# Kernel optimization log

Measured on AMD Instinct MI355X. Metric: run time of the kernel, lower is better.

The kernel has to match this reference:

```python
import jax, jax.numpy as jnp
import numpy as np

N, H, T, G = 4096, 64, 6, 16  # nodes, hidden, topk kvecs, graphs


def _rope(h, pos, kvecs, batch):
    # h: [N,H], pos: [N,3], kvecs: [G,T,3], batch: [N]
    phase = jnp.einsum('nc,ntc->nt', pos, kvecs[batch])      # [N,T]
    cos = jnp.cos(phase).T[:, :, None]                        # [T,N,1]
    sin = jnp.sin(phase).T[:, :, None]
    a, b = h[:, 0::2], h[:, 1::2]                             # [N,H/2] each
    rot_a = a[None] * cos - b[None] * sin                     # [T,N,H/2]
    rot_b = a[None] * sin + b[None] * cos
    return jnp.concatenate([rot_a, rot_b], axis=-1)           # [T,N,H]


def setup_inputs() -> dict:
    key = jax.random.key(0)
    ks = jax.random.split(key, 8)
    node_feat = jax.random.normal(ks[0], (N, H), dtype=jnp.float32)
    node_feat_sr = jax.random.normal(ks[1], (N, H), dtype=jnp.float32)
    positions = jax.random.uniform(ks[2], (N, 3), dtype=jnp.float32) * 12.0  # ~bulk-water box
    kvecs = jax.random.normal(ks[3], (G, T, 3), dtype=jnp.float32)
    batch = jnp.sort(jax.random.randint(ks[4], (N,), 0, G)).astype(jnp.int32)
    W_readout = jax.random.normal(ks[5], (H, H), dtype=jnp.float32) / np.sqrt(H)
    W_qkv = jax.random.normal(ks[6], (3 * H, H), dtype=jnp.float32) / np.sqrt(H)
    W_tp = jax.random.normal(ks[7], (H, H, H), dtype=jnp.float32) / H
    return {'node_feat': node_feat, 'node_feat_sr': node_feat_sr,
            'positions': positions, 'kvecs': kvecs, 'batch': batch,
            'W_readout': W_readout, 'W_qkv': W_qkv, 'W_tp': W_tp}


def reference(node_feat, node_feat_sr, positions, kvecs, batch, W_readout, W_qkv, W_tp):
    scale_q = 1.0 / np.sqrt(H)
    scalars = node_feat @ W_readout.T                         # linear_readout -> [N,H]
    qkv = scalars @ W_qkv.T                                   # [N,3H]
    q, k, v = qkv[:, :H], qkv[:, H:2 * H], qkv[:, 2 * H:]
    q, k = jax.nn.silu(q), jax.nn.silu(k)
    q = _rope(q, positions, kvecs, batch) * scale_q           # [T,N,H]
    k = _rope(k, positions, kvecs, batch)                     # [T,N,H]
    # per-node outer product k (x) v, scatter-summed per graph
    kv_node = k[:, :, :, None] * v[None, :, None, :]          # [T,N,H,H]
    kv_graph = jax.ops.segment_sum(kv_node.transpose(1, 0, 2, 3), batch,
                                   num_segments=G)            # [G,T,H,H]
    # beta[t,n,e] = sum_d q[t,n,d] * kv_graph[batch[n],t,d,e]; update = beta.sum(0)
    update = jnp.einsum('tnd,ntde->ne', q, kv_graph[batch])   # [N,H]
    # FullyConnectedTensorProduct(Hx0e, Hx0e -> Hx0e) == bilinear form
    node_nl = jnp.einsum('ni,nj,kij->nk', node_feat_sr, update, W_tp)
    return node_nl
```

## Files before the change

kernel.cpp:

```cpp
#include <hip/hip_runtime.h>

#define NN 4096
#define HH 64
#define TT 6
#define GG 16

constexpr int OFF_OFFS = 0;
constexpr int OFF_QS   = 32;
constexpr int OFF_KS   = OFF_QS + NN * HH;
constexpr int OFF_VS   = OFF_KS + NN * HH;
constexpr int OFF_COS  = OFF_VS + NN * HH;
constexpr int OFF_SIN  = OFF_COS + NN * 8;
constexpr int OFF_KVG  = OFF_SIN + NN * 8;
constexpr int OFF_UPD  = OFF_KVG + GG * TT * HH * HH;

typedef __bf16 bf16x8 __attribute__((ext_vector_type(8)));
typedef float f32x4 __attribute__((ext_vector_type(4)));

__global__ __launch_bounds__(256) void k_qkv(const float* __restrict__ feat,
                                             const float* __restrict__ pos,
                                             const float* __restrict__ kvecs,
                                             const int* __restrict__ batch,
                                             const float* __restrict__ Wro,
                                             const float* __restrict__ Wqkv,
                                             float* __restrict__ ws) {
    int tid = threadIdx.x, blk = blockIdx.x;
    if (blk == 256) {
        int g = tid;
        if (g <= GG) {
            int lo = 0, hi = NN;
            while (lo < hi) { int mid = (lo + hi) >> 1; if (batch[mid] < g) lo = mid + 1; else hi = mid; }
            ((int*)(ws + OFF_OFFS))[g] = lo;
        }
        return;
    }
    {
        float4 z = {0.f, 0.f, 0.f, 0.f};
        float4* kz = (float4*)(ws + OFF_KVG) + blk * 384;
        kz[tid] = z;
        if (tid < 128) kz[256 + tid] = z;
    }
    __shared__ float Wro_l[64][66];
    __shared__ float Wq_l[192][66];
    #pragma unroll
    for (int k = 0; k < 16; ++k) {
        int idx = k * 256 + tid;
        Wro_l[idx >> 6][idx & 63] = Wro[idx];
    }
    #pragma unroll
    for (int k = 0; k < 48; ++k) {
        int idx = k * 256 + tid;
        Wq_l[idx >> 6][idx & 63] = Wqkv[idx];
    }
    __syncthreads();
    int w = tid >> 6, j = tid & 63;
    float fl[4];
    #pragma unroll
    for (int mi = 0; mi < 4; ++mi) fl[mi] = feat[(blk * 16 + w * 4 + mi) * 64 + j];
    float scal[4] = {0.f, 0.f, 0.f, 0.f};
    #pragma unroll
    for (int i4 = 0; i4 < 16; ++i4) {
        float4 w4 = *(const float4*)&Wro_l[j][i4 * 4];
        #pragma unroll
        for (int mi = 0; mi < 4; ++mi) {
            scal[mi] += __shfl(fl[mi], i4 * 4 + 0, 64) * w4.x
                      + __shfl(fl[mi], i4 * 4 + 1, 64) * w4.y
                      + __shfl(fl[mi], i4 * 4 + 2, 64) * w4.z
                      + __shfl(fl[mi], i4 * 4 + 3, 64) * w4.w;
        }
    }
    float qa[4] = {0.f,0.f,0.f,0.f}, ka[4] = {0.f,0.f,0.f,0.f}, va[4] = {0.f,0.f,0.f,0.f};
    #pragma unroll
    for (int i4 = 0; i4 < 16; ++i4) {
        float4 wq = *(const float4*)&Wq_l[j][i4 * 4];
        float4 wk = *(const float4*)&Wq_l[64 + j][i4 * 4];
        float4 wv = *(const float4*)&Wq_l[128 + j][i4 * 4];
        #pragma unroll
        for (int mi = 0; mi < 4; ++mi) {
            float s0 = __shfl(scal[mi], i4 * 4 + 0, 64);
            float s1 = __shfl(scal[mi], i4 * 4 + 1, 64);
            float s2 = __shfl(scal[mi], i4 * 4 + 2, 64);
            float s3 = __shfl(scal[mi], i4 * 4 + 3, 64);
            qa[mi] += s0 * wq.x + s1 * wq.y + s2 * wq.z + s3 * wq.w;
            ka[mi] += s0 * wk.x + s1 * wk.y + s2 * wk.z + s3 * wk.w;
            va[mi] += s0 * wv.x + s1 * wv.y + s2 * wv.z + s3 * wv.w;
        }
    }
    #pragma unroll
    for (int mi = 0; mi < 4; ++mi) {
        int n = blk * 16 + w * 4 + mi;
        float q = qa[mi], kk2 = ka[mi], v = va[mi];
        float qs = q / (1.f + __expf(-q)) * 0.125f;
        float ks = kk2 / (1.f + __expf(-kk2));
        ws[OFF_QS + n * 64 + j] = qs;
        ws[OFF_KS + n * 64 + j] = ks;
        ws[OFF_VS + n * 64 + j] = v;
        if (j < 6) {
            int g = batch[n];
            const float* kv = &kvecs[(g * 6 + j) * 3];
            float ph = pos[n * 3 + 0] * kv[0] + pos[n * 3 + 1] * kv[1] + pos[n * 3 + 2] * kv[2];
            ws[OFF_COS + n * 8 + j] = cosf(ph);
            ws[OFF_SIN + n * 8 + j] = sinf(ph);
        }
    }
}

__global__ __launch_bounds__(256) void k_kvg(float* __restrict__ ws) {
    __shared__ float kr8[8][64];
    __shared__ float v8[8][64];
    int bid = blockIdx.x;
    int g = bid / 48, rem = bid % 48, t = rem >> 3, ch = rem & 7;
    const int* off = (const int*)(ws + OFF_OFFS);
    int n0 = off[g] + ch * 64;
    int n1 = min(off[g + 1], n0 + 64);
    if (n0 >= n1) return;
    int tid = threadIdx.x;
    int e = tid & 63, dg = tid >> 6;
    float acc[16];
    #pragma unroll
    for (int k = 0; k < 16; ++k) acc[k] = 0.f;
    for (int base = n0; base < n1; base += 8) {
        int cnt = min(8, n1 - base);
        #pragma unroll
        for (int half = 0; half < 2; ++half) {
            int idx = half * 256 + tid;
            int ns = idx >> 6, d = idx & 63;
            float kr = 0.f, vv = 0.f;
            if (ns < cnt) {
                int n = base + ns;
                float ka2 = ws[OFF_KS + n * 64 + 2 * (d & 31)];
                float kb = ws[OFF_KS + n * 64 + 2 * (d & 31) + 1];
                float c = ws[OFF_COS + n * 8 + t], s = ws[OFF_SIN + n * 8 + t];
                kr = (d < 32) ? (ka2 * c - kb * s) : (ka2 * s + kb * c);
                vv = ws[OFF_VS + n * 64 + d];
            }
            kr8[ns][d] = kr; v8[ns][d] = vv;
        }
        __syncthreads();
        #pragma unroll
        for (int ns = 0; ns < 8; ++ns) {
            float vv = v8[ns][e];
            const float4* kp = (const float4*)&kr8[ns][dg * 16];
            #pragma unroll
            for (int q4 = 0; q4 < 4; ++q4) {
                float4 kq = kp[q4];
                acc[q4 * 4 + 0] += kq.x * vv; acc[q4 * 4 + 1] += kq.y * vv;
                acc[q4 * 4 + 2] += kq.z * vv; acc[q4 * 4 + 3] += kq.w * vv;
            }
        }
        __syncthreads();
    }
    float* kvg = ws + OFF_KVG + ((g * 6 + t) * 64 + dg * 16) * 64;
    #pragma unroll
    for (int k = 0; k < 16; ++k) atomicAdd(&kvg[k * 64 + e], acc[k]);
}

__global__ __launch_bounds__(256) void k_upd(float* __restrict__ ws, float* __restrict__ out) {
    int tid = threadIdx.x, bid = blockIdx.x;
    ((float4*)out)[bid * 256 + tid] = (float4){0.f, 0.f, 0.f, 0.f};
    int g = bid >> 4, ch = bid & 15;
    const int* off = (const int*)(ws + OFF_OFFS);
    int n0 = off[g] + ch * 32;
    int nend = off[g + 1];
    if (n0 >= nend) return;
    int w = tid >> 6, lane = tid & 63;
    int wm = w & 1, wn = w >> 1;
    int lr = lane & 15, lg = lane >> 4;
    int nrow = n0 + wm * 16 + lr;
    int nc = min(nrow, nend - 1);
    float qv[16];
    const float* qsr = ws + OFF_QS + nc * 64 + lg * 16;
    #pragma unroll
    for (int u = 0; u < 4; ++u) *(float4*)&qv[u * 4] = *(const float4*)&qsr[u * 4];
    float cs[8], sn[8];
    *(float4*)&cs[0] = *(const float4*)(ws + OFF_COS + nc * 8);
    *(float4*)&cs[4] = *(const float4*)(ws + OFF_COS + nc * 8 + 4);
    *(float4*)&sn[0] = *(const float4*)(ws + OFF_SIN + nc * 8);
    *(float4*)&sn[4] = *(const float4*)(ws + OFF_SIN + nc * 8 + 4);
    const float* kvg = ws + OFF_KVG + g * (TT * HH * HH);
    int col0 = wn * 32 + lr, col1 = col0 + 16;
    f32x4 acc0 = {0.f,0.f,0.f,0.f}, acc1 = {0.f,0.f,0.f,0.f};
    #pragma unroll
    for (int kk = 0; kk < 12; ++kk) {
        int t = kk >> 1;
        float c = cs[t], s = sn[t];
        bf16x8 afr;
        #pragma unroll
        for (int ii = 0; ii < 8; ++ii) {
            float a = qv[2 * ii], b = qv[2 * ii + 1];
            float r = ((kk & 1) == 0) ? (a * c - b * s) : (a * s + b * c);
            afr[ii] = (__bf16)r;
        }
        const float* bp = kvg + (kk * 32 + lg * 8) * 64;
        bf16x8 b0, b1;
        #pragma unroll
        for (int i = 0; i < 8; ++i) {
            b0[i] = (__bf16)bp[i * 64 + col0];
            b1[i] = (__bf16)bp[i * 64 + col1];
        }
        acc0 = __builtin_amdgcn_mfma_f32_16x16x32_bf16(afr, b0, acc0, 0, 0, 0);
        acc1 = __builtin_amdgcn_mfma_f32_16x16x32_bf16(afr, b1, acc1, 0, 0, 0);
    }
    #pragma unroll
    for (int r = 0; r < 4; ++r) {
        int n = n0 + wm * 16 + lg * 4 + r;
        if (n < nend) {
            ws[OFF_UPD + n * 64 + col0] = acc0[r];
            ws[OFF_UPD + n * 64 + col1] = acc1[r];
        }
    }
}

__device__ __forceinline__ bf16x8 make_afrag(const float* p, float s) {
    float4 u0 = *(const float4*)p;
    float4 u1 = *(const float4*)(p + 4);
    bf16x8 r;
    r[0] = (__bf16)(s * u0.x); r[1] = (__bf16)(s * u0.y); r[2] = (__bf16)(s * u0.z); r[3] = (__bf16)(s * u0.w);
    r[4] = (__bf16)(s * u1.x); r[5] = (__bf16)(s * u1.y); r[6] = (__bf16)(s * u1.z); r[7] = (__bf16)(s * u1.w);
    return r;
}
__device__ __forceinline__ bf16x8 make_bfrag(const float* p) {
    float4 u0 = *(const float4*)p;
    float4 u1 = *(const float4*)(p + 4);
    bf16x8 r;
    r[0] = (__bf16)u0.x; r[1] = (__bf16)u0.y; r[2] = (__bf16)u0.z; r[3] = (__bf16)u0.w;
    r[4] = (__bf16)u1.x; r[5] = (__bf16)u1.y; r[6] = (__bf16)u1.z; r[7] = (__bf16)u1.w;
    return r;
}

__global__ __launch_bounds__(256) void k_out(const float* __restrict__ sr,
                                             const float* __restrict__ Wtp,
                                             const float* __restrict__ ws,
                                             float* __restrict__ out) {
    __shared__ float sr_l[64][65];
    __shared__ float up_l[64][68];
    __shared__ float w_l[64][68];
    int tid = threadIdx.x;
    int mb = blockIdx.x & 63, kspl = blockIdx.x >> 6;
    int m0 = mb * 64;
    #pragma unroll
    for (int k = 0; k < 16; ++k) {
        int idx = k * 256 + tid;
        int m = idx >> 6, c = idx & 63;
        sr_l[m][c] = sr[(m0 + m) * 64 + c];
        up_l[m][c] = ws[OFF_UPD + (m0 + m) * 64 + c];
    }
    __syncthreads();
    int w = tid >> 6, lane = tid & 63;
    int wm = w >> 1, wn = w & 1;
    int lr = lane & 15, lg = lane >> 4;
    f32x4 acc[2][2];
    #pragma unroll
    for (int a = 0; a < 2; ++a)
        #pragma unroll
        for (int b = 0; b < 2; ++b) acc[a][b] = (f32x4){0.f, 0.f, 0.f, 0.f};

    for (int ii = 0; ii < 8; ++ii) {
        int i = kspl * 8 + ii;
        #pragma unroll
        for (int k = 0; k < 4; ++k) {
            int idx = k * 256 + tid;
            int col = idx >> 4, j4 = (idx & 15) * 4;
            float4 wv = *(const float4*)&Wtp[(col * 64 + i) * 64 + j4];
            *(float4*)&w_l[col][j4] = wv;
        }
        __syncthreads();
        float s0 = sr_l[wm * 32 + lr][i];
        float s1 = sr_l[wm * 32 + 16 + lr][i];
        #pragma unroll
        for (int kc = 0; kc < 2; ++kc) {
            int j0 = kc * 32 + lg * 8;
            bf16x8 a0 = make_afrag(&up_l[wm * 32 + lr][j0], s0);
            bf16x8 a1 = make_afrag(&up_l[wm * 32 + 16 + lr][j0], s1);
            bf16x8 b0 = make_bfrag(&w_l[wn * 32 + lr][j0]);
            bf16x8 b1 = make_bfrag(&w_l[wn * 32 + 16 + lr][j0]);
            acc[0][0] = __builtin_amdgcn_mfma_f32_16x16x32_bf16(a0, b0, acc[0][0], 0, 0, 0);
            acc[0][1] = __builtin_amdgcn_mfma_f32_16x16x32_bf16(a0, b1, acc[0][1], 0, 0, 0);
            acc[1][0] = __builtin_amdgcn_mfma_f32_16x16x32_bf16(a1, b0, acc[1][0], 0, 0, 0);
            acc[1][1] = __builtin_amdgcn_mfma_f32_16x16x32_bf16(a1, b1, acc[1][1], 0, 0, 0);
        }
        __syncthreads();
    }
    #pragma unroll
    for (int mt = 0; mt < 2; ++mt)
        #pragma unroll
        for (int nt = 0; nt < 2; ++nt) {
            int row = m0 + wm * 32 + mt * 16 + lg * 4;
            int col = wn * 32 + nt * 16 + lr;
            #pragma unroll
            for (int r = 0; r < 4; ++r)
                atomicAdd(&out[(row + r) * 64 + col], acc[mt][nt][r]);
        }
}

extern "C" void kernel_launch(void* const* d_in, const int* in_sizes, int n_in,
                              void* d_out, int out_size, void* d_ws, size_t ws_size,
                              hipStream_t stream) {
    const float* node_feat    = (const float*)d_in[0];
    const float* node_feat_sr = (const float*)d_in[1];
    const float* positions    = (const float*)d_in[2];
    const float* kvecs        = (const float*)d_in[3];
    const int*   batch        = (const int*)d_in[4];
    const float* W_readout    = (const float*)d_in[5];
    const float* W_qkv        = (const float*)d_in[6];
    const float* W_tp         = (const float*)d_in[7];
    float* out = (float*)d_out;
    float* ws  = (float*)d_ws;

    k_qkv<<<257, 256, 0, stream>>>(node_feat, positions, kvecs, batch, W_readout, W_qkv, ws);
    k_kvg<<<768, 256, 0, stream>>>(ws);
    k_upd<<<256, 256, 0, stream>>>(ws, out);
    k_out<<<512, 256, 0, stream>>>(node_feat_sr, W_tp, ws, out);
}
```

Measured before the change: 126.1 us.

## Rebalance grid sizes across kernels and move output zeroing into kvg kernel

Doubles the k_qkv grid so each block handles 8 nodes instead of 16, and halves the KV-graph zeroing per block to match. k_upd now uses 16-node chunks with one MFMA tile per wave, giving twice as many blocks, and k_out halves its block count by giving each block twice as many i-slices. Output zeroing moves from k_upd into k_kvg. The aim is better occupancy and load balance in the early kernels and fewer atomics in k_out. The cost is re-staging the weights into shared memory in more blocks and longer serial loops in k_out.

```diff
diff --git a/kernel.cpp b/kernel.cpp
--- a/kernel.cpp
+++ b/kernel.cpp
@@ -25,7 +25,7 @@
                                              const float* __restrict__ Wqkv,
                                              float* __restrict__ ws) {
     int tid = threadIdx.x, blk = blockIdx.x;
-    if (blk == 256) {
+    if (blk == 512) {
         int g = tid;
         if (g <= GG) {
             int lo = 0, hi = NN;
@@ -34,11 +34,9 @@
         }
         return;
     }
-    {
-        float4 z = {0.f, 0.f, 0.f, 0.f};
-        float4* kz = (float4*)(ws + OFF_KVG) + blk * 384;
-        kz[tid] = z;
-        if (tid < 128) kz[256 + tid] = z;
+    if (tid < 192) {
+        float4* kz = (float4*)(ws + OFF_KVG) + blk * 192;
+        kz[tid] = (float4){0.f, 0.f, 0.f, 0.f};
     }
     __shared__ float Wro_l[64][66];
     __shared__ float Wq_l[192][66];
@@ -54,29 +52,29 @@
     }
     __syncthreads();
     int w = tid >> 6, j = tid & 63;
-    float fl[4];
-    #pragma unroll
-    for (int mi = 0; mi < 4; ++mi) fl[mi] = feat[(blk * 16 + w * 4 + mi) * 64 + j];
-    float scal[4] = {0.f, 0.f, 0.f, 0.f};
+    float fl[2];
+    #pragma unroll
+    for (int mi = 0; mi < 2; ++mi) fl[mi] = feat[(blk * 8 + w * 2 + mi) * 64 + j];
+    float scal[2] = {0.f, 0.f};
     #pragma unroll
     for (int i4 = 0; i4 < 16; ++i4) {
         float4 w4 = *(const float4*)&Wro_l[j][i4 * 4];
         #pragma unroll
-        for (int mi = 0; mi < 4; ++mi) {
+        for (int mi = 0; mi < 2; ++mi) {
             scal[mi] += __shfl(fl[mi], i4 * 4 + 0, 64) * w4.x
                       + __shfl(fl[mi], i4 * 4 + 1, 64) * w4.y
                       + __shfl(fl[mi], i4 * 4 + 2, 64) * w4.z
                       + __shfl(fl[mi], i4 * 4 + 3, 64) * w4.w;
         }
     }
-    float qa[4] = {0.f,0.f,0.f,0.f}, ka[4] = {0.f,0.f,0.f,0.f}, va[4] = {0.f,0.f,0.f,0.f};
+    float qa[2] = {0.f,0.f}, ka[2] = {0.f,0.f}, va[2] = {0.f,0.f};
     #pragma unroll
     for (int i4 = 0; i4 < 16; ++i4) {
         float4 wq = *(const float4*)&Wq_l[j][i4 * 4];
         float4 wk = *(const float4*)&Wq_l[64 + j][i4 * 4];
         float4 wv = *(const float4*)&Wq_l[128 + j][i4 * 4];
         #pragma unroll
-        for (int mi = 0; mi < 4; ++mi) {
+        for (int mi = 0; mi < 2; ++mi) {
             float s0 = __shfl(scal[mi], i4 * 4 + 0, 64);
             float s1 = __shfl(scal[mi], i4 * 4 + 1, 64);
             float s2 = __shfl(scal[mi], i4 * 4 + 2, 64);
@@ -87,8 +85,8 @@
         }
     }
     #pragma unroll
-    for (int mi = 0; mi < 4; ++mi) {
-        int n = blk * 16 + w * 4 + mi;
+    for (int mi = 0; mi < 2; ++mi) {
+        int n = blk * 8 + w * 2 + mi;
         float q = qa[mi], kk2 = ka[mi], v = va[mi];
         float qs = q / (1.f + __expf(-q)) * 0.125f;
         float ks = kk2 / (1.f + __expf(-kk2));
@@ -105,16 +103,19 @@
     }
 }
 
-__global__ __launch_bounds__(256) void k_kvg(float* __restrict__ ws) {
+__global__ __launch_bounds__(256) void k_kvg(float* __restrict__ ws, float* __restrict__ out) {
     __shared__ float kr8[8][64];
     __shared__ float v8[8][64];
     int bid = blockIdx.x;
+    int tid = threadIdx.x;
+    if (bid < 256) {
+        ((float4*)out)[bid * 256 + tid] = (float4){0.f, 0.f, 0.f, 0.f};
+    }
     int g = bid / 48, rem = bid % 48, t = rem >> 3, ch = rem & 7;
     const int* off = (const int*)(ws + OFF_OFFS);
     int n0 = off[g] + ch * 64;
     int n1 = min(off[g + 1], n0 + 64);
     if (n0 >= n1) return;
-    int tid = threadIdx.x;
     int e = tid & 63, dg = tid >> 6;
     float acc[16];
     #pragma unroll
@@ -155,18 +156,16 @@
     for (int k = 0; k < 16; ++k) atomicAdd(&kvg[k * 64 + e], acc[k]);
 }
 
-__global__ __launch_bounds__(256) void k_upd(float* __restrict__ ws, float* __restrict__ out) {
+__global__ __launch_bounds__(256) void k_upd(float* __restrict__ ws) {
     int tid = threadIdx.x, bid = blockIdx.x;
-    ((float4*)out)[bid * 256 + tid] = (float4){0.f, 0.f, 0.f, 0.f};
-    int g = bid >> 4, ch = bid & 15;
+    int g = bid >> 5, ch = bid & 31;
     const int* off = (const int*)(ws + OFF_OFFS);
-    int n0 = off[g] + ch * 32;
+    int n0 = off[g] + ch * 16;
     int nend = off[g + 1];
     if (n0 >= nend) return;
     int w = tid >> 6, lane = tid & 63;
-    int wm = w & 1, wn = w >> 1;
     int lr = lane & 15, lg = lane >> 4;
-    int nrow = n0 + wm * 16 + lr;
+    int nrow = n0 + lr;
     int nc = min(nrow, nend - 1);
     float qv[16];
     const float* qsr = ws + OFF_QS + nc * 64 + lg * 16;
@@ -178,8 +177,8 @@
     *(float4*)&sn[0] = *(const float4*)(ws + OFF_SIN + nc * 8);
     *(float4*)&sn[4] = *(const float4*)(ws + OFF_SIN + nc * 8 + 4);
     const float* kvg = ws + OFF_KVG + g * (TT * HH * HH);
-    int col0 = wn * 32 + lr, col1 = col0 + 16;
-    f32x4 acc0 = {0.f,0.f,0.f,0.f}, acc1 = {0.f,0.f,0.f,0.f};
+    int col0 = w * 16 + lr;
+    f32x4 acc0 = {0.f,0.f,0.f,0.f};
     #pragma unroll
     for (int kk = 0; kk < 12; ++kk) {
         int t = kk >> 1;
@@ -192,22 +191,15 @@
             afr[ii] = (__bf16)r;
         }
         const float* bp = kvg + (kk * 32 + lg * 8) * 64;
-        bf16x8 b0, b1;
-        #pragma unroll
-        for (int i = 0; i < 8; ++i) {
-            b0[i] = (__bf16)bp[i * 64 + col0];
-            b1[i] = (__bf16)bp[i * 64 + col1];
-        }
+        bf16x8 b0;
+        #pragma unroll
+        for (int i = 0; i < 8; ++i) b0[i] = (__bf16)bp[i * 64 + col0];
         acc0 = __builtin_amdgcn_mfma_f32_16x16x32_bf16(afr, b0, acc0, 0, 0, 0);
-        acc1 = __builtin_amdgcn_mfma_f32_16x16x32_bf16(afr, b1, acc1, 0, 0, 0);
     }
     #pragma unroll
     for (int r = 0; r < 4; ++r) {
-        int n = n0 + wm * 16 + lg * 4 + r;
-        if (n < nend) {
-            ws[OFF_UPD + n * 64 + col0] = acc0[r];
-            ws[OFF_UPD + n * 64 + col1] = acc1[r];
-        }
+        int n = n0 + lg * 4 + r;
+        if (n < nend) ws[OFF_UPD + n * 64 + col0] = acc0[r];
     }
 }
 
@@ -255,8 +247,8 @@
         #pragma unroll
         for (int b = 0; b < 2; ++b) acc[a][b] = (f32x4){0.f, 0.f, 0.f, 0.f};
 
-    for (int ii = 0; ii < 8; ++ii) {
-        int i = kspl * 8 + ii;
+    for (int ii = 0; ii < 16; ++ii) {
+        int i = kspl * 16 + ii;
         #pragma unroll
         for (int k = 0; k < 4; ++k) {
             int idx = k * 256 + tid;
@@ -307,8 +299,8 @@
     float* out = (float*)d_out;
     float* ws  = (float*)d_ws;
 
-    k_qkv<<<257, 256, 0, stream>>>(node_feat, positions, kvecs, batch, W_readout, W_qkv, ws);
-    k_kvg<<<768, 256, 0, stream>>>(ws);
-    k_upd<<<256, 256, 0, stream>>>(ws, out);
-    k_out<<<512, 256, 0, stream>>>(node_feat_sr, W_tp, ws, out);
-}
+    k_qkv<<<513, 256, 0, stream>>>(node_feat, positions, kvecs, batch, W_readout, W_qkv, ws);
+    k_kvg<<<768, 256, 0, stream>>>(ws, out);
+    k_upd<<<512, 256, 0, stream>>>(ws);
+    k_out<<<256, 256, 0, stream>>>(node_feat_sr, W_tp, ws, out);
+}
```

Result: slower. 129.9 us (+2.9%).

## Fuse four stages into one cooperative kernel with grid syncs

Applied to the files above, without the earlier changes.

Merges the qkv, kv-graph, update and output stages into a single cooperative kernel with 256 blocks, separated by grid-wide barriers, and keeps the separate launches as a fallback. Shared memory is unioned across phases. Work is redistributed: each block handles several kvg units, the update stage uses single-MFMA units, and the output stage uses fewer blocks with a larger k-split. Weights are staged as fp16 in LDS. The aim is to remove inter-kernel launch gaps, but grid syncs add cost, the later stages get less parallelism, and fp16 weights lose some precision.

```diff
diff --git a/kernel.cpp b/kernel.cpp
--- a/kernel.cpp
+++ b/kernel.cpp
@@ -1,9 +1,17 @@
 #include <hip/hip_runtime.h>
+#include <hip/hip_cooperative_groups.h>
+
+namespace cg = cooperative_groups;
 
 #define NN 4096
 #define HH 64
 #define TT 6
 #define GG 16
+#define NBLK 256
+
+typedef __bf16 bf16x8 __attribute__((ext_vector_type(8)));
+typedef float f32x4 __attribute__((ext_vector_type(4)));
+typedef _Float16 h4 __attribute__((ext_vector_type(4)));
 
 constexpr int OFF_OFFS = 0;
 constexpr int OFF_QS   = 32;
@@ -14,43 +22,64 @@
 constexpr int OFF_KVG  = OFF_SIN + NN * 8;
 constexpr int OFF_UPD  = OFF_KVG + GG * TT * HH * HH;
 
-typedef __bf16 bf16x8 __attribute__((ext_vector_type(8)));
-typedef float f32x4 __attribute__((ext_vector_type(4)));
-
-__global__ __launch_bounds__(256) void k_qkv(const float* __restrict__ feat,
-                                             const float* __restrict__ pos,
-                                             const float* __restrict__ kvecs,
-                                             const int* __restrict__ batch,
-                                             const float* __restrict__ Wro,
-                                             const float* __restrict__ Wqkv,
-                                             float* __restrict__ ws) {
-    int tid = threadIdx.x, blk = blockIdx.x;
-    if (blk == 256) {
-        int g = tid;
-        if (g <= GG) {
-            int lo = 0, hi = NN;
-            while (lo < hi) { int mid = (lo + hi) >> 1; if (batch[mid] < g) lo = mid + 1; else hi = mid; }
-            ((int*)(ws + OFF_OFFS))[g] = lo;
-        }
-        return;
+struct P1Sm { _Float16 WroH[64 * 66]; _Float16 WqH[192 * 66]; };
+struct P2Sm { float kr[8][64]; float v[8][64]; };
+struct P4Sm { float sr[64][65]; float up[64][68]; float w[64][68]; };
+union SMemU { P1Sm p1; P2Sm p2; P4Sm p4; };
+
+__device__ __forceinline__ bf16x8 make_afrag(const float* p, float s) {
+    float4 u0 = *(const float4*)p;
+    float4 u1 = *(const float4*)(p + 4);
+    bf16x8 r;
+    r[0] = (__bf16)(s * u0.x); r[1] = (__bf16)(s * u0.y); r[2] = (__bf16)(s * u0.z); r[3] = (__bf16)(s * u0.w);
+    r[4] = (__bf16)(s * u1.x); r[5] = (__bf16)(s * u1.y); r[6] = (__bf16)(s * u1.z); r[7] = (__bf16)(s * u1.w);
+    return r;
+}
+__device__ __forceinline__ bf16x8 make_bfrag(const float* p) {
+    float4 u0 = *(const float4*)p;
+    float4 u1 = *(const float4*)(p + 4);
+    bf16x8 r;
+    r[0] = (__bf16)u0.x; r[1] = (__bf16)u0.y; r[2] = (__bf16)u0.z; r[3] = (__bf16)u0.w;
+    r[4] = (__bf16)u1.x; r[5] = (__bf16)u1.y; r[6] = (__bf16)u1.z; r[7] = (__bf16)u1.w;
+    return r;
+}
+
+__device__ __forceinline__ void p1_body(P1Sm& sm, int tid, int blk,
+                                        const float* __restrict__ feat,
+                                        const float* __restrict__ pos,
+                                        const float* __restrict__ kvecs,
+                                        const int* __restrict__ batch,
+                                        const float* __restrict__ Wro,
+                                        const float* __restrict__ Wqkv,
+                                        float* __restrict__ ws,
+                                        float* __restrict__ out) {
+    if (blk == 0 && tid <= GG) {
+        int g = tid, lo = 0, hi = NN;
+        while (lo < hi) { int mid = (lo + hi) >> 1; if (batch[mid] < g) lo = mid + 1; else hi = mid; }
+        ((int*)(ws + OFF_OFFS))[g] = lo;
     }
     {
         float4 z = {0.f, 0.f, 0.f, 0.f};
         float4* kz = (float4*)(ws + OFF_KVG) + blk * 384;
         kz[tid] = z;
         if (tid < 128) kz[256 + tid] = z;
-    }
-    __shared__ float Wro_l[64][66];
-    __shared__ float Wq_l[192][66];
-    #pragma unroll
-    for (int k = 0; k < 16; ++k) {
-        int idx = k * 256 + tid;
-        Wro_l[idx >> 6][idx & 63] = Wro[idx];
-    }
-    #pragma unroll
-    for (int k = 0; k < 48; ++k) {
-        int idx = k * 256 + tid;
-        Wq_l[idx >> 6][idx & 63] = Wqkv[idx];
+        ((float4*)out)[blk * 256 + tid] = z;
+    }
+    #pragma unroll
+    for (int k = 0; k < 8; ++k) {
+        int e2 = k * 256 + tid;
+        float2 v = ((const float2*)Wro)[e2];
+        int r = e2 >> 5, c2 = e2 & 31;
+        _Float16* dst = &sm.WroH[r * 66 + c2 * 2];
+        dst[0] = (_Float16)v.x; dst[1] = (_Float16)v.y;
+    }
+    #pragma unroll
+    for (int k = 0; k < 24; ++k) {
+        int e2 = k * 256 + tid;
+        float2 v = ((const float2*)Wqkv)[e2];
+        int r = e2 >> 5, c2 = e2 & 31;
+        _Float16* dst = &sm.WqH[r * 66 + c2 * 2];
+        dst[0] = (_Float16)v.x; dst[1] = (_Float16)v.y;
     }
     __syncthreads();
     int w = tid >> 6, j = tid & 63;
@@ -60,30 +89,31 @@
     float scal[4] = {0.f, 0.f, 0.f, 0.f};
     #pragma unroll
     for (int i4 = 0; i4 < 16; ++i4) {
-        float4 w4 = *(const float4*)&Wro_l[j][i4 * 4];
+        h4 w4 = *(const h4*)&sm.WroH[j * 66 + i4 * 4];
+        float w0 = (float)w4[0], w1 = (float)w4[1], w2 = (float)w4[2], w3 = (float)w4[3];
         #pragma unroll
         for (int mi = 0; mi < 4; ++mi) {
-            scal[mi] += __shfl(fl[mi], i4 * 4 + 0, 64) * w4.x
-                      + __shfl(fl[mi], i4 * 4 + 1, 64) * w4.y
-                      + __shfl(fl[mi], i4 * 4 + 2, 64) * w4.z
-                      + __shfl(fl[mi], i4 * 4 + 3, 64) * w4.w;
+            scal[mi] += __shfl(fl[mi], i4 * 4 + 0, 64) * w0
+                      + __shfl(fl[mi], i4 * 4 + 1, 64) * w1
+                      + __shfl(fl[mi], i4 * 4 + 2, 64) * w2
+                      + __shfl(fl[mi], i4 * 4 + 3, 64) * w3;
         }
     }
     float qa[4] = {0.f,0.f,0.f,0.f}, ka[4] = {0.f,0.f,0.f,0.f}, va[4] = {0.f,0.f,0.f,0.f};
     #pragma unroll
     for (int i4 = 0; i4 < 16; ++i4) {
-        float4 wq = *(const float4*)&Wq_l[j][i4 * 4];
-        float4 wk = *(const float4*)&Wq_l[64 + j][i4 * 4];
-        float4 wv = *(const float4*)&Wq_l[128 + j][i4 * 4];
+        h4 hq = *(const h4*)&sm.WqH[j * 66 + i4 * 4];
+        h4 hk = *(const h4*)&sm.WqH[(64 + j) * 66 + i4 * 4];
+        h4 hv = *(const h4*)&sm.WqH[(128 + j) * 66 + i4 * 4];
         #pragma unroll
         for (int mi = 0; mi < 4; ++mi) {
             float s0 = __shfl(scal[mi], i4 * 4 + 0, 64);
             float s1 = __shfl(scal[mi], i4 * 4 + 1, 64);
             float s2 = __shfl(scal[mi], i4 * 4 + 2, 64);
             float s3 = __shfl(scal[mi], i4 * 4 + 3, 64);
-            qa[mi] += s0 * wq.x + s1 * wq.y + s2 * wq.z + s3 * wq.w;
-            ka[mi] += s0 * wk.x + s1 * wk.y + s2 * wk.z + s3 * wk.w;
-            va[mi] += s0 * wv.x + s1 * wv.y + s2 * wv.z + s3 * wv.w;
+            qa[mi] += s0 * (float)hq[0] + s1 * (float)hq[1] + s2 * (float)hq[2] + s3 * (float)hq[3];
+            ka[mi] += s0 * (float)hk[0] + s1 * (float)hk[1] + s2 * (float)hk[2] + s3 * (float)hk[3];
+            va[mi] += s0 * (float)hv[0] + s1 * (float)hv[1] + s2 * (float)hv[2] + s3 * (float)hv[3];
         }
     }
     #pragma unroll
@@ -105,16 +135,12 @@
     }
 }
 
-__global__ __launch_bounds__(256) void k_kvg(float* __restrict__ ws) {
-    __shared__ float kr8[8][64];
-    __shared__ float v8[8][64];
-    int bid = blockIdx.x;
-    int g = bid / 48, rem = bid % 48, t = rem >> 3, ch = rem & 7;
+__device__ __forceinline__ void p2_body(P2Sm& sm, int tid, int u, float* __restrict__ ws) {
     const int* off = (const int*)(ws + OFF_OFFS);
+    int g = u / 48, rem = u % 48, t = rem >> 3, ch = rem & 7;
     int n0 = off[g] + ch * 64;
     int n1 = min(off[g + 1], n0 + 64);
     if (n0 >= n1) return;
-    int tid = threadIdx.x;
     int e = tid & 63, dg = tid >> 6;
     float acc[16];
     #pragma unroll
@@ -134,13 +160,13 @@
                 kr = (d < 32) ? (ka2 * c - kb * s) : (ka2 * s + kb * c);
                 vv = ws[OFF_VS + n * 64 + d];
             }
-            kr8[ns][d] = kr; v8[ns][d] = vv;
+            sm.kr[ns][d] = kr; sm.v[ns][d] = vv;
         }
         __syncthreads();
         #pragma unroll
         for (int ns = 0; ns < 8; ++ns) {
-            float vv = v8[ns][e];
-            const float4* kp = (const float4*)&kr8[ns][dg * 16];
+            float vv = sm.v[ns][e];
+            const float4* kp = (const float4*)&sm.kr[ns][dg * 16];
             #pragma unroll
             for (int q4 = 0; q4 < 4; ++q4) {
                 float4 kq = kp[q4];
@@ -155,31 +181,26 @@
     for (int k = 0; k < 16; ++k) atomicAdd(&kvg[k * 64 + e], acc[k]);
 }
 
-__global__ __launch_bounds__(256) void k_upd(float* __restrict__ ws, float* __restrict__ out) {
-    int tid = threadIdx.x, bid = blockIdx.x;
-    ((float4*)out)[bid * 256 + tid] = (float4){0.f, 0.f, 0.f, 0.f};
-    int g = bid >> 4, ch = bid & 15;
+__device__ __forceinline__ void p3_body(int tid, int u, float* __restrict__ ws) {
     const int* off = (const int*)(ws + OFF_OFFS);
-    int n0 = off[g] + ch * 32;
+    int g = u >> 5, ch = u & 31;
+    int n0 = off[g] + ch * 16;
     int nend = off[g + 1];
     if (n0 >= nend) return;
-    int w = tid >> 6, lane = tid & 63;
-    int wm = w & 1, wn = w >> 1;
-    int lr = lane & 15, lg = lane >> 4;
-    int nrow = n0 + wm * 16 + lr;
-    int nc = min(nrow, nend - 1);
+    int w = tid >> 6, lane = tid & 63, lr = lane & 15, lg = lane >> 4;
+    int nc = min(n0 + lr, nend - 1);
     float qv[16];
     const float* qsr = ws + OFF_QS + nc * 64 + lg * 16;
     #pragma unroll
-    for (int u = 0; u < 4; ++u) *(float4*)&qv[u * 4] = *(const float4*)&qsr[u * 4];
+    for (int u2 = 0; u2 < 4; ++u2) *(float4*)&qv[u2 * 4] = *(const float4*)&qsr[u2 * 4];
     float cs[8], sn[8];
     *(float4*)&cs[0] = *(const float4*)(ws + OFF_COS + nc * 8);
     *(float4*)&cs[4] = *(const float4*)(ws + OFF_COS + nc * 8 + 4);
     *(float4*)&sn[0] = *(const float4*)(ws + OFF_SIN + nc * 8);
     *(float4*)&sn[4] = *(const float4*)(ws + OFF_SIN + nc * 8 + 4);
     const float* kvg = ws + OFF_KVG + g * (TT * HH * HH);
-    int col0 = wn * 32 + lr, col1 = col0 + 16;
-    f32x4 acc0 = {0.f,0.f,0.f,0.f}, acc1 = {0.f,0.f,0.f,0.f};
+    int col0 = w * 16 + lr;
+    f32x4 acc0 = {0.f, 0.f, 0.f, 0.f};
     #pragma unroll
     for (int kk = 0; kk < 12; ++kk) {
         int t = kk >> 1;
@@ -188,62 +209,35 @@
         #pragma unroll
         for (int ii = 0; ii < 8; ++ii) {
             float a = qv[2 * ii], b = qv[2 * ii + 1];
-            float r = ((kk & 1) == 0) ? (a * c - b * s) : (a * s + b * c);
-            afr[ii] = (__bf16)r;
+            float rr = ((kk & 1) == 0) ? (a * c - b * s) : (a * s + b * c);
+            afr[ii] = (__bf16)rr;
         }
         const float* bp = kvg + (kk * 32 + lg * 8) * 64;
-        bf16x8 b0, b1;
-        #pragma unroll
-        for (int i = 0; i < 8; ++i) {
-            b0[i] = (__bf16)bp[i * 64 + col0];
-            b1[i] = (__bf16)bp[i * 64 + col1];
-        }
+        bf16x8 b0;
+        #pragma unroll
+        for (int i = 0; i < 8; ++i) b0[i] = (__bf16)bp[i * 64 + col0];
         acc0 = __builtin_amdgcn_mfma_f32_16x16x32_bf16(afr, b0, acc0, 0, 0, 0);
-        acc1 = __builtin_amdgcn_mfma_f32_16x16x32_bf16(afr, b1, acc1, 0, 0, 0);
     }
     #pragma unroll
     for (int r = 0; r < 4; ++r) {
-        int n = n0 + wm * 16 + lg * 4 + r;
-        if (n < nend) {
-            ws[OFF_UPD + n * 64 + col0] = acc0[r];
-            ws[OFF_UPD + n * 64 + col1] = acc1[r];
-        }
-    }
-}
-
-__device__ __forceinline__ bf16x8 make_afrag(const float* p, float s) {
-    float4 u0 = *(const float4*)p;
-    float4 u1 = *(const float4*)(p + 4);
-    bf16x8 r;
-    r[0] = (__bf16)(s * u0.x); r[1] = (__bf16)(s * u0.y); r[2] = (__bf16)(s * u0.z); r[3] = (__bf16)(s * u0.w);
-    r[4] = (__bf16)(s * u1.x); r[5] = (__bf16)(s * u1.y); r[6] = (__bf16)(s * u1.z); r[7] = (__bf16)(s * u1.w);
-    return r;
-}
-__device__ __forceinline__ bf16x8 make_bfrag(const float* p) {
-    float4 u0 = *(const float4*)p;
-    float4 u1 = *(const float4*)(p + 4);
-    bf16x8 r;
-    r[0] = (__bf16)u0.x; r[1] = (__bf16)u0.y; r[2] = (__bf16)u0.z; r[3] = (__bf16)u0.w;
-    r[4] = (__bf16)u1.x; r[5] = (__bf16)u1.y; r[6] = (__bf16)u1.z; r[7] = (__bf16)u1.w;
-    return r;
-}
-
-__global__ __launch_bounds__(256) void k_out(const float* __restrict__ sr,
-                                             const float* __restrict__ Wtp,
-                                             const float* __restrict__ ws,
-                                             float* __restrict__ out) {
-    __shared__ float sr_l[64][65];
-    __shared__ float up_l[64][68];
-    __shared__ float w_l[64][68];
-    int tid = threadIdx.x;
-    int mb = blockIdx.x & 63, kspl = blockIdx.x >> 6;
+        int n = n0 + lg * 4 + r;
+        if (n < nend) ws[OFF_UPD + n * 64 + col0] = acc0[r];
+    }
+}
+
+__device__ __forceinline__ void p4_body(P4Sm& sm, int tid, int blk,
+                                        const float* __restrict__ srf,
+                                        const float* __restrict__ Wtp,
+                                        float* __restrict__ ws,
+                                        float* __restrict__ out) {
+    int mb = blk & 63, kspl = blk >> 6;
     int m0 = mb * 64;
     #pragma unroll
     for (int k = 0; k < 16; ++k) {
         int idx = k * 256 + tid;
         int m = idx >> 6, c = idx & 63;
-        sr_l[m][c] = sr[(m0 + m) * 64 + c];
-        up_l[m][c] = ws[OFF_UPD + (m0 + m) * 64 + c];
+        sm.sr[m][c] = srf[(m0 + m) * 64 + c];
+        sm.up[m][c] = ws[OFF_UPD + (m0 + m) * 64 + c];
     }
     __syncthreads();
     int w = tid >> 6, lane = tid & 63;
@@ -255,25 +249,25 @@
         #pragma unroll
         for (int b = 0; b < 2; ++b) acc[a][b] = (f32x4){0.f, 0.f, 0.f, 0.f};
 
-    for (int ii = 0; ii < 8; ++ii) {
-        int i = kspl * 8 + ii;
+    for (int ii = 0; ii < 16; ++ii) {
+        int i = kspl * 16 + ii;
         #pragma unroll
         for (int k = 0; k < 4; ++k) {
             int idx = k * 256 + tid;
             int col = idx >> 4, j4 = (idx & 15) * 4;
             float4 wv = *(const float4*)&Wtp[(col * 64 + i) * 64 + j4];
-            *(float4*)&w_l[col][j4] = wv;
-        }
-        __syncthreads();
-        float s0 = sr_l[wm * 32 + lr][i];
-        float s1 = sr_l[wm * 32 + 16 + lr][i];
+            *(float4*)&sm.w[col][j4] = wv;
+        }
+        __syncthreads();
+        float s0 = sm.sr[wm * 32 + lr][i];
+        float s1 = sm.sr[wm * 32 + 16 + lr][i];
         #pragma unroll
         for (int kc = 0; kc < 2; ++kc) {
             int j0 = kc * 32 + lg * 8;
-            bf16x8 a0 = make_afrag(&up_l[wm * 32 + lr][j0], s0);
-            bf16x8 a1 = make_afrag(&up_l[wm * 32 + 16 + lr][j0], s1);
-            bf16x8 b0 = make_bfrag(&w_l[wn * 32 + lr][j0]);
-            bf16x8 b1 = make_bfrag(&w_l[wn * 32 + 16 + lr][j0]);
+            bf16x8 a0 = make_afrag(&sm.up[wm * 32 + lr][j0], s0);
+            bf16x8 a1 = make_afrag(&sm.up[wm * 32 + 16 + lr][j0], s1);
+            bf16x8 b0 = make_bfrag(&sm.w[wn * 32 + lr][j0]);
+            bf16x8 b1 = make_bfrag(&sm.w[wn * 32 + 16 + lr][j0]);
             acc[0][0] = __builtin_amdgcn_mfma_f32_16x16x32_bf16(a0, b0, acc[0][0], 0, 0, 0);
             acc[0][1] = __builtin_amdgcn_mfma_f32_16x16x32_bf16(a0, b1, acc[0][1], 0, 0, 0);
             acc[1][0] = __builtin_amdgcn_mfma_f32_16x16x32_bf16(a1, b0, acc[1][0], 0, 0, 0);
@@ -291,6 +285,63 @@
             for (int r = 0; r < 4; ++r)
                 atomicAdd(&out[(row + r) * 64 + col], acc[mt][nt][r]);
         }
+}
+
+__device__ __forceinline__ void gsync(cg::grid_group& g) {
+    __threadfence();
+    g.sync();
+    __threadfence();
+}
+
+__global__ __launch_bounds__(256) void k_fused(const float* __restrict__ feat,
+                                               const float* __restrict__ srf,
+                                               const float* __restrict__ pos,
+                                               const float* __restrict__ kvecs,
+                                               const int* __restrict__ batch,
+                                               const float* __restrict__ Wro,
+                                               const float* __restrict__ Wqkv,
+                                               const float* __restrict__ Wtp,
+                                               float* __restrict__ ws,
+                                               float* __restrict__ out) {
+    __shared__ SMemU sm;
+    cg::grid_group grid = cg::this_grid();
+    int tid = threadIdx.x, blk = blockIdx.x;
+    p1_body(sm.p1, tid, blk, feat, pos, kvecs, batch, Wro, Wqkv, ws, out);
+    gsync(grid);
+    for (int r = 0; r < 3; ++r) {
+        p2_body(sm.p2, tid, blk * 3 + r, ws);
+        __syncthreads();
+    }
+    gsync(grid);
+    for (int r = 0; r < 2; ++r) p3_body(tid, blk * 2 + r, ws);
+    gsync(grid);
+    p4_body(sm.p4, tid, blk, srf, Wtp, ws, out);
+}
+
+__global__ __launch_bounds__(256) void k_p1(const float* __restrict__ feat,
+                                            const float* __restrict__ pos,
+                                            const float* __restrict__ kvecs,
+                                            const int* __restrict__ batch,
+                                            const float* __restrict__ Wro,
+                                            const float* __restrict__ Wqkv,
+                                            float* __restrict__ ws,
+                                            float* __restrict__ out) {
+    __shared__ P1Sm sm;
+    p1_body(sm, threadIdx.x, blockIdx.x, feat, pos, kvecs, batch, Wro, Wqkv, ws, out);
+}
+__global__ __launch_bounds__(256) void k_p2(float* __restrict__ ws) {
+    __shared__ P2Sm sm;
+    p2_body(sm, threadIdx.x, blockIdx.x, ws);
+}
+__global__ __launch_bounds__(256) void k_p3(float* __restrict__ ws) {
+    p3_body(threadIdx.x, blockIdx.x, ws);
+}
+__global__ __launch_bounds__(256) void k_p4(const float* __restrict__ srf,
+                                            const float* __restrict__ Wtp,
+                                            float* __restrict__ ws,
+                                            float* __restrict__ out) {
+    __shared__ P4Sm sm;
+    p4_body(sm, threadIdx.x, blockIdx.x, srf, Wtp, ws, out);
 }
 
 extern "C" void kernel_launch(void* const* d_in, const int* in_sizes, int n_in,
@@ -307,8 +358,16 @@
     float* out = (float*)d_out;
     float* ws  = (float*)d_ws;
 
-    k_qkv<<<257, 256, 0, stream>>>(node_feat, positions, kvecs, batch, W_readout, W_qkv, ws);
-    k_kvg<<<768, 256, 0, stream>>>(ws);
-    k_upd<<<256, 256, 0, stream>>>(ws, out);
-    k_out<<<512, 256, 0, stream>>>(node_feat_sr, W_tp, ws, out);
-}
+    void* args[] = {(void*)&node_feat, (void*)&node_feat_sr, (void*)&positions,
+                    (void*)&kvecs, (void*)&batch, (void*)&W_readout, (void*)&W_qkv,
+                    (void*)&W_tp, (void*)&ws, (void*)&out};
+    hipError_t err = hipLaunchCooperativeKernel((const void*)k_fused, dim3(NBLK), dim3(256),
+                                                args, 0, stream);
+    if (err != hipSuccess) {
+        k_p1<<<NBLK, 256, 0, stream>>>(node_feat, positions, kvecs, batch,
+                                       W_readout, W_qkv, ws, out);
+        k_p2<<<768, 256, 0, stream>>>(ws);
+        k_p3<<<512, 256, 0, stream>>>(ws);
+        k_p4<<<NBLK, 256, 0, stream>>>(node_feat_sr, W_tp, ws, out);
+    }
+}
```

Result: slower. 354.3 us (+180.8%).
